# Optimization experiments

Measured on AMD Instinct MI355X. Metric: run time of the kernel, lower is better.

Reference implementation:

```python
import jax, jax.numpy as jnp
import numpy as np
from jax import lax

B, T, C = 4, 2048, 2048
HK, HV = 16, 16
DK, DV = 128, 128
KW = 4  # conv kernel width
KEY_DIM = HK * DK      # 2048
VAL_DIM = HV * DV      # 2048
QKV_DIM = 2 * KEY_DIM + VAL_DIM  # 6144
EPS_RMS = 1e-6
EPS_NORM = 1e-12


def setup_inputs() -> dict:
    key = jax.random.key(0)
    ks = jax.random.split(key, 7)
    s = 0.02
    x = jax.random.normal(ks[0], (B, T, C), dtype=jnp.float32)
    positions = jnp.broadcast_to(jnp.arange(T, dtype=jnp.int64 if jax.config.jax_enable_x64 else jnp.int32), (B, T))
    W_qkvz = jax.random.normal(ks[1], (C, QKV_DIM + VAL_DIM), dtype=jnp.float32) * s
    W_b = jax.random.normal(ks[2], (C, HV), dtype=jnp.float32) * s
    W_a = jax.random.normal(ks[3], (C, HV), dtype=jnp.float32) * s
    conv_w = jax.random.normal(ks[4], (QKV_DIM, 1, KW), dtype=jnp.float32) * 0.1
    norm_w = jnp.ones((DV,), dtype=jnp.float32)
    W_out = jax.random.normal(ks[5], (VAL_DIM, C), dtype=jnp.float32) * s
    return {"x": x, "positions": positions, "W_qkvz": W_qkvz, "W_b": W_b,
            "W_a": W_a, "conv_w": conv_w, "norm_w": norm_w, "W_out": W_out}


def _l2norm(u):
    n = jnp.sqrt(jnp.sum(u * u, axis=-1, keepdims=True))
    return u / jnp.maximum(n, EPS_NORM)


def _forward(x, W_qkvz, W_b, W_a, conv_w, norm_w, W_out):
    qkvz = x @ W_qkvz                               # [B,T,QKV+VAL]
    qkv, z = qkvz[..., :QKV_DIM], qkvz[..., QKV_DIM:]
    z = z.reshape(B, T, HV, DV)
    beta = jax.nn.sigmoid(x @ W_b)                  # [B,T,HV]
    alpha = jax.nn.sigmoid(x @ W_a)                 # [B,T,HV]

    # depthwise causal conv1d (padding K-1 then truncate to T)
    xc = jnp.transpose(qkv, (0, 2, 1))              # [B,QKV_DIM,T]
    xc = lax.conv_general_dilated(xc, conv_w, window_strides=(1,),
                                  padding=[(KW - 1, 0)],
                                  feature_group_count=QKV_DIM,
                                  dimension_numbers=("NCH", "OIH", "NCH"))
    qkv = jnp.transpose(jax.nn.silu(xc), (0, 2, 1))  # [B,T,QKV_DIM]

    q = _l2norm(qkv[..., :KEY_DIM].reshape(B, T, HK, DK))
    k = _l2norm(qkv[..., KEY_DIM:2 * KEY_DIM].reshape(B, T, HK, DK))
    v = qkv[..., 2 * KEY_DIM:].reshape(B, T, HV, DV)

    def step(state, inp):
        q_t, k_t, v_t, b_t, a_t = inp               # [B,H,DK],[B,H,DK],[B,H,DV],[B,H],[B,H]
        state = a_t[:, :, None, None] * state + \
                b_t[:, :, None, None] * (k_t[..., :, None] * v_t[:, :, None, :])
        out = jnp.einsum('bhk,bhkv->bhv', q_t, state)
        return state, out

    state0 = jnp.zeros((B, HK, DK, DV), dtype=x.dtype)
    seq = (jnp.moveaxis(q, 1, 0), jnp.moveaxis(k, 1, 0), jnp.moveaxis(v, 1, 0),
           jnp.moveaxis(beta, 1, 0), jnp.moveaxis(alpha, 1, 0))
    _, outs = lax.scan(step, state0, seq)           # [T,B,H,DV]
    out = jnp.moveaxis(outs, 0, 1)                  # [B,T,H,DV]

    # RMSNorm over head_v_dim (fp32), gated by sigmoid(z)
    of = out.astype(jnp.float32)
    rms = jnp.mean(of * of, axis=-1, keepdims=True)
    out = ((of * lax.rsqrt(rms + EPS_RMS)) * norm_w).astype(out.dtype)
    out = out * jax.nn.sigmoid(z)
    return out.reshape(B, T, VAL_DIM) @ W_out


def reference(x, positions, W_qkvz, W_b, W_a, conv_w, norm_w, W_out):
    return _forward(x, W_qkvz, W_b, W_a, conv_w, norm_w, W_out)
```

## Files before the change

kernel.cpp:

```cpp
#include <hip/hip_runtime.h>
#include <hip/hip_bf16.h>

typedef __bf16 bf16_t;
typedef __attribute__((ext_vector_type(8))) __bf16 bf16x8;
typedef __attribute__((ext_vector_type(4))) float floatx4;


__device__ __forceinline__ void gload16(const void* g, void* l) {
  __builtin_amdgcn_global_load_lds(
      (const __attribute__((address_space(1))) void*)g,
      (__attribute__((address_space(3))) void*)l, 16, 0, 0);
}

__global__ __launch_bounds__(256) void k_cast_bf16(const float* __restrict__ in,
                                                   bf16_t* __restrict__ out) {
  long i = ((long)blockIdx.x * 256 + threadIdx.x) * 8;
  const float4 a = *(const float4*)(in + i);
  const float4 b = *(const float4*)(in + i + 4);
  bf16x8 o;
  o[0] = (bf16_t)a.x; o[1] = (bf16_t)a.y; o[2] = (bf16_t)a.z; o[3] = (bf16_t)a.w;
  o[4] = (bf16_t)b.x; o[5] = (bf16_t)b.y; o[6] = (bf16_t)b.z; o[7] = (bf16_t)b.w;
  *(bf16x8*)(out + i) = o;
}

__global__ void k_transpose_cast(const float* __restrict__ in, bf16_t* __restrict__ out,
                                 int R, int Ccols) {
  __shared__ float tile[32][33];
  int c0 = blockIdx.x * 32, r0 = blockIdx.y * 32;
  for (int i = threadIdx.y; i < 32; i += 8)
    tile[i][threadIdx.x] = in[(long)(r0 + i) * Ccols + c0 + threadIdx.x];
  __syncthreads();
  for (int i = threadIdx.y; i < 32; i += 8)
    out[(long)(c0 + i) * R + r0 + threadIdx.x] = (bf16_t)tile[threadIdx.x][i];
}

__global__ void k_transpose_f32(const float* __restrict__ in, float* __restrict__ out,
                                int R, int Ccols) {
  int r = blockIdx.x * blockDim.x + threadIdx.x;
  if (r < R)
    for (int c = 0; c < Ccols; ++c) out[(long)c * R + r] = in[(long)r * Ccols + c];
}

__global__ __launch_bounds__(256) void k_beta_alpha(const float* __restrict__ x,
                                                    const float* __restrict__ WbT,
                                                    const float* __restrict__ WaT,
                                                    float* __restrict__ beta,
                                                    float* __restrict__ alpha) {
  extern __shared__ float xs[];
  const long row0 = (long)blockIdx.x * 16;
  const int tid = threadIdx.x;
  {
    const float4* src = (const float4*)(x + row0 * 2048);
    float4* dst = (float4*)xs;
    for (int i = tid; i < 16 * 512; i += 256) dst[i] = src[i];
  }
  __syncthreads();
  const int wv = tid >> 6, lane = tid & 63;
  for (int oo = 0; oo < 8; ++oo) {
    const int o = wv * 8 + oo;
    const float* Wrow = (o < 16) ? (WbT + (long)o * 2048) : (WaT + (long)(o - 16) * 2048);
    float acc[16];
#pragma unroll
    for (int r = 0; r < 16; ++r) acc[r] = 0.f;
    for (int kc = 0; kc < 8; ++kc) {
      const float4 w4 = *(const float4*)(Wrow + kc * 256 + lane * 4);
#pragma unroll
      for (int r = 0; r < 16; ++r) {
        const float4 xv = *(const float4*)&xs[r * 2048 + kc * 256 + lane * 4];
        acc[r] += w4.x * xv.x + w4.y * xv.y + w4.z * xv.z + w4.w * xv.w;
      }
    }
#pragma unroll
    for (int r = 0; r < 16; ++r) {
      float s = acc[r];
      for (int off = 32; off; off >>= 1) s += __shfl_down(s, off);
      if (lane == 0) {
        const long row = row0 + r;
        const int b = (int)(row >> 11), t = (int)(row & 2047);
        const float sig = 1.f / (1.f + __expf(-s));
        float* dst = (o < 16) ? beta : alpha;
        dst[((long)(b * 16 + (o & 15))) * 2048 + t] = sig;
      }
    }
  }
}

template <typename OUT_T>
__global__ __launch_bounds__(512, 2) void k_gemm256(const bf16_t* __restrict__ A,
                                                    const bf16_t* __restrict__ Bt,
                                                    OUT_T* __restrict__ C,
                                                    int N, int K, int lda) {
  extern __shared__ char gsm[];
  const int m0 = blockIdx.y * 256, n0 = blockIdx.x * 256;
  const int tid = threadIdx.x;
  const int w = tid >> 6, l = tid & 63;
  const int wm = w >> 2, wn = w & 3;
  const int l15 = l & 15, lg = l >> 4;

  const bf16_t* asrc[4];
  const bf16_t* bsrc[4];
  int dofs[4];
#pragma unroll
  for (int t = 0; t < 4; ++t) {
    int c = t * 512 + tid;
    int row = c >> 3, cs = (c & 7) ^ (row & 7);
    asrc[t] = A + (long)(m0 + row) * lda + cs * 8;
    bsrc[t] = Bt + (long)(n0 + row) * K + cs * 8;
    dofs[t] = c * 16;
  }

  auto STAGE = [&](int buf, int k0) {
    char* ab = gsm + buf * 65536;
    char* bb = ab + 32768;
#pragma unroll
    for (int t = 0; t < 4; ++t) {
      gload16(asrc[t] + k0, ab + dofs[t]);
      gload16(bsrc[t] + k0, bb + dofs[t]);
    }
  };

  floatx4 acc[8][4] = {};
  STAGE(0, 0);
  const int NK = K >> 6;
  for (int kt = 0; kt < NK; ++kt) {
    __syncthreads();
    if (kt + 1 < NK) STAGE((kt + 1) & 1, (kt + 1) << 6);
    const char* As_ = gsm + (kt & 1) * 65536;
    const char* Bs_ = As_ + 32768;
#pragma unroll
    for (int ks = 0; ks < 2; ++ks) {
      bf16x8 af[8], bfr[4];
#pragma unroll
      for (int mi = 0; mi < 8; ++mi) {
        const int r = wm * 128 + mi * 16 + l15;
        af[mi] = *(const bf16x8*)(As_ + r * 128 + ((((ks << 2) + lg) ^ (r & 7)) << 4));
      }
#pragma unroll
      for (int ni = 0; ni < 4; ++ni) {
        const int r = wn * 64 + ni * 16 + l15;
        bfr[ni] = *(const bf16x8*)(Bs_ + r * 128 + ((((ks << 2) + lg) ^ (r & 7)) << 4));
      }
      __builtin_amdgcn_s_setprio(1);
#pragma unroll
      for (int mi = 0; mi < 8; ++mi)
#pragma unroll
        for (int ni = 0; ni < 4; ++ni)
          acc[mi][ni] = __builtin_amdgcn_mfma_f32_16x16x32_bf16(af[mi], bfr[ni], acc[mi][ni], 0, 0, 0);
      __builtin_amdgcn_s_setprio(0);
    }
  }
  const int crow0 = m0 + wm * 128 + lg * 4;
  const int ccol = n0 + wn * 64 + l15;
#pragma unroll
  for (int mi = 0; mi < 8; ++mi)
#pragma unroll
    for (int ni = 0; ni < 4; ++ni)
#pragma unroll
      for (int r = 0; r < 4; ++r)
        C[(long)(crow0 + mi * 16 + r) * N + ccol + ni * 16] = (OUT_T)acc[mi][ni][r];
}

__global__ __launch_bounds__(256) void k_conv(const bf16_t* __restrict__ qkvz,
                                              const float* __restrict__ conv_w,
                                              bf16_t* __restrict__ q, bf16_t* __restrict__ k,
                                              bf16_t* __restrict__ v) {
  int row = blockIdx.x;
  int b = row >> 11, t = row & 2047;
  __shared__ float ys[6144];
  __shared__ float gsum[32][9];
  __shared__ float norms[32];
  const int c0 = threadIdx.x * 8;
  for (int c8 = c0; c8 < 6144; c8 += 2048) {
    bf16x8 xr[4];
#pragma unroll
    for (int w2 = 0; w2 < 4; ++w2) {
      int tt = t - 3 + w2;
      bf16x8 zr = {};
      xr[w2] = (tt >= 0) ? *(const bf16x8*)&qkvz[((long)(b * 2048 + tt)) * 8192 + c8] : zr;
    }
#pragma unroll
    for (int j = 0; j < 8; ++j) {
      float4 wv = *(const float4*)&conv_w[(c8 + j) * 4];
      float a = (float)xr[0][j] * wv.x + (float)xr[1][j] * wv.y +
                (float)xr[2][j] * wv.z + (float)xr[3][j] * wv.w;
      ys[c8 + j] = a / (1.f + __expf(-a));
    }
  }
  __syncthreads();
  {
    int g = threadIdx.x >> 3, j = threadIdx.x & 7;
    float s = 0.f;
#pragma unroll
    for (int e = 0; e < 16; ++e) {
      float yv = ys[g * 128 + j * 16 + e];
      s += yv * yv;
    }
    gsum[g][j] = s;
  }
  __syncthreads();
  if (threadIdx.x < 32) {
    float s = 0.f;
#pragma unroll
    for (int j = 0; j < 8; j++) s += gsum[threadIdx.x][j];
    norms[threadIdx.x] = 1.f / fmaxf(sqrtf(s), 1e-12f);
  }
  __syncthreads();
  for (int c8 = c0; c8 < 6144; c8 += 2048) {
    float scale;
    bf16_t* dst;
    if (c8 < 2048) {
      int h = c8 >> 7;
      scale = norms[h];
      dst = q + (((long)(b * 16 + h)) * 2048 + t) * 128 + (c8 & 127);
    } else if (c8 < 4096) {
      int h = (c8 - 2048) >> 7;
      scale = norms[16 + h];
      dst = k + (((long)(b * 16 + h)) * 2048 + t) * 128 + (c8 & 127);
    } else {
      scale = 1.f;
      int h = (c8 - 4096) >> 7;
      dst = v + (((long)(b * 16 + h)) * 2048 + t) * 128 + (c8 & 127);
    }
    bf16x8 o;
#pragma unroll
    for (int j = 0; j < 8; ++j) o[j] = (bf16_t)(ys[c8 + j] * scale);
    *(bf16x8*)dst = o;
  }
}

__global__ __launch_bounds__(256) void k_tr_kv(const bf16_t* __restrict__ kv,
                                               const bf16_t* __restrict__ vv,
                                               bf16_t* __restrict__ qkvz) {
  __shared__ bf16_t t_lds[64 * 136];
  int bh = blockIdx.x >> 5, tc = blockIdx.x & 31;
  int t0 = tc * 64;
  int tid = threadIdx.x;
#pragma unroll
  for (int pass = 0; pass < 2; ++pass) {
    const bf16_t* src = (pass == 0 ? kv : vv) + (long)bh * 2048 * 128 + (long)t0 * 128;
    int r = tid >> 2, sc = (tid & 3) * 32;
    bf16x8 x0 = *(const bf16x8*)(src + (long)r * 128 + sc);
    bf16x8 x1 = *(const bf16x8*)(src + (long)r * 128 + sc + 8);
    bf16x8 x2 = *(const bf16x8*)(src + (long)r * 128 + sc + 16);
    bf16x8 x3 = *(const bf16x8*)(src + (long)r * 128 + sc + 24);
    __syncthreads();
    *(bf16x8*)&t_lds[r * 136 + sc] = x0;
    *(bf16x8*)&t_lds[r * 136 + sc + 8] = x1;
    *(bf16x8*)&t_lds[r * 136 + sc + 16] = x2;
    *(bf16x8*)&t_lds[r * 136 + sc + 24] = x3;
    __syncthreads();
    int d = tid >> 1, h2 = tid & 1;
    bf16_t* dst = qkvz + (long)(bh * 128 + d) * 8192 + (pass ? 4096 : 2048) + t0 + h2 * 32;
#pragma unroll
    for (int g = 0; g < 4; ++g) {
      bf16x8 o;
#pragma unroll
      for (int j = 0; j < 8; ++j) o[j] = t_lds[(h2 * 32 + g * 8 + j) * 136 + d];
      *(bf16x8*)(dst + g * 8) = o;
    }
  }
}

__global__ __launch_bounds__(512, 1) void k_scan_chunked(
    const bf16_t* __restrict__ qv, const bf16_t* __restrict__ kv,
    bf16_t* __restrict__ qkvz, float* __restrict__ so_hi,
    const float* __restrict__ beta, const float* __restrict__ alpha) {
  extern __shared__ char smem[];
  bf16_t* q_lds = (bf16_t*)smem;
  bf16_t* kn_lds = q_lds + 8704;
  bf16_t* kT_lds = kn_lds + 8704;
  bf16_t* vT_lds = kT_lds + 9216;
  bf16_t* P_lds = vT_lds + 2304;
  bf16_t* St_lds = P_lds + 4608;
  float* G_lds = (float*)(St_lds + 4352);
  float* bet_lds = G_lds + 64;
  float* w_lds = bet_lds + 64;
  float* eG_lds = w_lds + 64;

  const int bh = blockIdx.x, dvb = blockIdx.y;
  const int b = bh >> 4, h = bh & 15;
  const int tid = threadIdx.x;
  const int w = tid >> 6, l = tid & 63;
  const int l15 = l & 15, lg = l >> 4;
  const int g = w & 1, r = w >> 1;

  const bf16_t* qb = qv + (long)bh * 2048 * 128;
  const bf16_t* kb = kv + (long)bh * 2048 * 128;
  const bf16_t* kTg = qkvz + (long)bh * 128 * 8192 + 2048;
  const bf16_t* vTg = qkvz + (long)(bh * 128 + dvb * 32) * 8192 + 4096;
  const float* bet = beta + (long)bh * 2048;
  const float* alp = alpha + (long)bh * 2048;

  floatx4 streg[2] = {};
  for (int i = tid; i < 2176; i += 512) ((float*)St_lds)[i] = 0.f;
  __syncthreads();

  const int sr = tid >> 3, ssc = (tid & 7) * 16;
  const int sdk = tid >> 2, ssc2 = (tid & 3) * 16;
  const int svr = tid >> 3, svc = (tid & 7) * 8;

  bf16x8 ra0, ra1, rb0, rb1, rc0, rc1, rd0 = {};
  float rbet = 0.f, ralp = 1.f;
  {
    const bf16_t* qs = qb + (long)sr * 128 + ssc;
    const bf16_t* ks = kb + (long)sr * 128 + ssc;
    const bf16_t* kts = kTg + (long)sdk * 8192 + ssc2;
    ra0 = *(const bf16x8*)qs; ra1 = *(const bf16x8*)(qs + 8);
    rb0 = *(const bf16x8*)ks; rb1 = *(const bf16x8*)(ks + 8);
    rc0 = *(const bf16x8*)kts; rc1 = *(const bf16x8*)(kts + 8);
    if (tid < 256) rd0 = *(const bf16x8*)(vTg + (long)svr * 8192 + svc);
    if (w == 0) { rbet = bet[l]; ralp = alp[l]; }
  }

  for (int c = 0; c < 32; ++c) {
    const int t0 = c * 64;
    {
      *(bf16x8*)&q_lds[sr * 136 + ssc] = ra0;
      *(bf16x8*)&q_lds[sr * 136 + ssc + 8] = ra1;
      *(bf16x8*)&kn_lds[sr * 136 + ssc] = rb0;
      *(bf16x8*)&kn_lds[sr * 136 + ssc + 8] = rb1;
      *(bf16x8*)&kT_lds[sdk * 72 + ssc2] = rc0;
      *(bf16x8*)&kT_lds[sdk * 72 + ssc2 + 8] = rc1;
      if (tid < 256) *(bf16x8*)&vT_lds[svr * 72 + svc] = rd0;
      if (w == 0) {
        float bsv = rbet;
        float la = __logf(ralp);
#pragma unroll
        for (int off = 1; off < 64; off <<= 1) {
          float xup = __shfl_up(la, off);
          if (l >= off) la += xup;
        }
        float ge = __shfl(la, 63);
        G_lds[l] = la;
        bet_lds[l] = bsv;
        w_lds[l] = bsv * __expf(ge - la);
        eG_lds[l] = __expf(la);
      }
    }
    __syncthreads();

    if (c + 1 < 32) {
      const int t1 = t0 + 64;
      const bf16_t* qs = qb + (long)(t1 + sr) * 128 + ssc;
      const bf16_t* ks = kb + (long)(t1 + sr) * 128 + ssc;
      const bf16_t* kts = kTg + (long)sdk * 8192 + t1 + ssc2;
      ra0 = *(const bf16x8*)qs; ra1 = *(const bf16x8*)(qs + 8);
      rb0 = *(const bf16x8*)ks; rb1 = *(const bf16x8*)(ks + 8);
      rc0 = *(const bf16x8*)kts; rc1 = *(const bf16x8*)(kts + 8);
      if (tid < 256) rd0 = *(const bf16x8*)(vTg + (long)svr * 8192 + t1 + svc);
      if (w == 0) { rbet = bet[t1 + l]; ralp = alp[t1 + l]; }
    }

    {
      bf16_t* p = &kT_lds[sdk * 72 + ssc2];
      bf16x8 x0 = *(bf16x8*)p, x1 = *(bf16x8*)(p + 8);
#pragma unroll
      for (int j = 0; j < 8; j++) {
        x0[j] = (bf16_t)((float)x0[j] * w_lds[ssc2 + j]);
        x1[j] = (bf16_t)((float)x1[j] * w_lds[ssc2 + 8 + j]);
      }
      *(bf16x8*)p = x0;
      *(bf16x8*)(p + 8) = x1;
    }

    {
      const int mi = w >> 1;
      bf16x8 aq[4];
#pragma unroll
      for (int ks = 0; ks < 4; ks++)
        aq[ks] = *(bf16x8*)&q_lds[(mi * 16 + l15) * 136 + ks * 32 + lg * 8];
#pragma unroll
      for (int sn2 = 0; sn2 < 2; sn2++) {
        const int sn = (w & 1) * 2 + sn2;
        floatx4 sc_ = {0.f, 0.f, 0.f, 0.f};
#pragma unroll
        for (int ks = 0; ks < 4; ks++) {
          bf16x8 bk = *(bf16x8*)&kn_lds[(sn * 16 + l15) * 136 + ks * 32 + lg * 8];
          sc_ = __builtin_amdgcn_mfma_f32_16x16x32_bf16(aq[ks], bk, sc_, 0, 0, 0);
        }
        const int sl = sn * 16 + l15;
        const float gs = G_lds[sl], bs = bet_lds[sl];
#pragma unroll
        for (int rr = 0; rr < 4; rr++) {
          const int tl = mi * 16 + lg * 4 + rr;
          float val = (sl <= tl) ? sc_[rr] * __expf(G_lds[tl] - gs) * bs : 0.f;
          P_lds[tl * 72 + sl] = (bf16_t)val;
        }
      }
    }
    __syncthreads();

    floatx4 acco = {0.f, 0.f, 0.f, 0.f};
    {
      const int rloc = g * 16 + l15;
      bf16x8 av0 = *(bf16x8*)&vT_lds[rloc * 72 + lg * 8];
      bf16x8 av1 = *(bf16x8*)&vT_lds[rloc * 72 + 32 + lg * 8];
      floatx4 f = {0.f, 0.f, 0.f, 0.f};
#pragma unroll
      for (int ks = 0; ks < 4; ks++) {
        bf16x8 aq = *(bf16x8*)&q_lds[(r * 16 + l15) * 136 + ks * 32 + lg * 8];
        bf16x8 bs_ = *(bf16x8*)&St_lds[rloc * 136 + ks * 32 + lg * 8];
        f = __builtin_amdgcn_mfma_f32_16x16x32_bf16(aq, bs_, f, 0, 0, 0);
      }
#pragma unroll
      for (int rr = 0; rr < 4; rr++) f[rr] *= eG_lds[r * 16 + lg * 4 + rr];
#pragma unroll
      for (int ks2 = 0; ks2 < 2; ks2++) {
        bf16x8 ap = *(bf16x8*)&P_lds[(r * 16 + l15) * 72 + ks2 * 32 + lg * 8];
        f = __builtin_amdgcn_mfma_f32_16x16x32_bf16(ap, (ks2 == 0) ? av0 : av1, f, 0, 0, 0);
      }
      acco = f;
      const float dcv = eG_lds[63];
#pragma unroll
      for (int ni = 0; ni < 2; ni++) {
        const int ni2 = r * 2 + ni;
#pragma unroll
        for (int rr = 0; rr < 4; rr++) streg[ni][rr] *= dcv;
        bf16x8 bk0 = *(bf16x8*)&kT_lds[(ni2 * 16 + l15) * 72 + lg * 8];
        bf16x8 bk1 = *(bf16x8*)&kT_lds[(ni2 * 16 + l15) * 72 + 32 + lg * 8];
        streg[ni] = __builtin_amdgcn_mfma_f32_16x16x32_bf16(av0, bk0, streg[ni], 0, 0, 0);
        streg[ni] = __builtin_amdgcn_mfma_f32_16x16x32_bf16(av1, bk1, streg[ni], 0, 0, 0);
      }
    }
    __syncthreads();

#pragma unroll
    for (int ni = 0; ni < 2; ni++) {
      const int ni2 = r * 2 + ni;
#pragma unroll
      for (int rr = 0; rr < 4; rr++)
        St_lds[(g * 16 + lg * 4 + rr) * 136 + ni2 * 16 + l15] = (bf16_t)streg[ni][rr];
    }
    {
      const int dvg = dvb * 32 + g * 16 + l15;
      const int hcol = h * 128 + dvg;
#pragma unroll
      for (int rr = 0; rr < 4; rr++) {
        const int t = t0 + r * 16 + lg * 4 + rr;
        const long row = (long)b * 2048 + t;
        if (hcol < 1024)
          ((float*)qkvz)[row * 4096 + hcol] = acco[rr];
        else
          so_hi[row * 1024 + hcol - 1024] = acco[rr];
      }
    }
  }
}

__global__ __launch_bounds__(256) void k_rmsgate(const float* __restrict__ so_hi,
                                                 const bf16_t* __restrict__ qkvz,
                                                 bf16_t* __restrict__ A2,
                                                 const float* __restrict__ norm_w) {
  long row = blockIdx.x;
  int tid = threadIdx.x;
  int h = tid >> 4, j = tid & 15;
  const float* srow = (h < 8) ? (const float*)qkvz + row * 4096 + h * 128 + j * 8
                              : so_hi + row * 1024 + (h - 8) * 128 + j * 8;
  float xv[8];
  *(float4*)&xv[0] = *(const float4*)srow;
  *(float4*)&xv[4] = *(const float4*)(srow + 4);
  float ss = 0.f;
#pragma unroll
  for (int e = 0; e < 8; e++) ss += xv[e] * xv[e];
  ss += __shfl_xor(ss, 1); ss += __shfl_xor(ss, 2);
  ss += __shfl_xor(ss, 4); ss += __shfl_xor(ss, 8);
  float rinv = rsqrtf(ss * (1.0f / 128.0f) + 1e-6f);
  const bf16_t* zrow = qkvz + row * 8192 + 6144 + h * 128 + j * 8;
  bf16x8 zv = *(const bf16x8*)zrow;
  bf16x8 o;
#pragma unroll
  for (int e = 0; e < 8; e++) {
    float z = (float)zv[e];
    float gate = 1.f / (1.f + __expf(-z));
    o[e] = (bf16_t)(xv[e] * rinv * norm_w[j * 8 + e] * gate);
  }
  *(bf16x8*)(A2 + row * 2048 + h * 128 + j * 8) = o;
}

extern "C" void kernel_launch(void* const* d_in, const int* in_sizes, int n_in,
                              void* d_out, int out_size, void* d_ws, size_t ws_size,
                              hipStream_t stream) {
  const float* x      = (const float*)d_in[0];
  const float* W_qkvz = (const float*)d_in[2];
  const float* W_b    = (const float*)d_in[3];
  const float* W_a    = (const float*)d_in[4];
  const float* conv_w = (const float*)d_in[5];
  const float* norm_w = (const float*)d_in[6];
  const float* W_out  = (const float*)d_in[7];
  float* out = (float*)d_out;
  char* ws = (char*)d_ws;

  bf16_t* qkvz  = (bf16_t*)(ws + 0);
  bf16_t* xb    = (bf16_t*)(ws + 134217728);
  bf16_t* qv    = (bf16_t*)(ws + 134217728);
  bf16_t* A2    = (bf16_t*)(ws + 134217728);
  bf16_t* WqT   = (bf16_t*)(ws + 167772160);
  bf16_t* kv    = (bf16_t*)(ws + 167772160);
  bf16_t* vv    = (bf16_t*)(ws + 201326592);
  float*  so_hi = (float*)(ws + 201326592);
  bf16_t* WoT   = (bf16_t*)(ws + 234881024);
  float*  WbT   = (float*)(ws + 243269632);
  float*  WaT   = (float*)(ws + 243400704);
  float*  beta  = (float*)(ws + 243531776);
  float*  alpha = (float*)(ws + 244056064);

  if (ws_size < 244580352) return;

  k_cast_bf16<<<8192, 256, 0, stream>>>(x, xb);
  k_transpose_cast<<<dim3(8192 / 32, 2048 / 32), dim3(32, 8), 0, stream>>>(W_qkvz, WqT, 2048, 8192);
  k_transpose_cast<<<dim3(2048 / 32, 2048 / 32), dim3(32, 8), 0, stream>>>(W_out, WoT, 2048, 2048);
  k_transpose_f32<<<8, 256, 0, stream>>>(W_b, WbT, 2048, 16);
  k_transpose_f32<<<8, 256, 0, stream>>>(W_a, WaT, 2048, 16);
  k_beta_alpha<<<512, 256, 131072, stream>>>(x, WbT, WaT, beta, alpha);
  k_gemm256<bf16_t><<<dim3(32, 32), 512, 131072, stream>>>(xb, WqT, qkvz, 8192, 2048, 2048);
  k_conv<<<8192, 256, 0, stream>>>(qkvz, conv_w, qv, kv, vv);
  k_tr_kv<<<2048, 256, 0, stream>>>(kv, vv, qkvz);
  k_scan_chunked<<<dim3(64, 4), 512, 76800, stream>>>(qv, kv, qkvz, so_hi, beta, alpha);
  k_rmsgate<<<8192, 256, 0, stream>>>(so_hi, qkvz, A2, norm_w);
  k_gemm256<float><<<dim3(8, 32), 512, 131072, stream>>>(A2, WoT, out, 2048, 2048, 2048);
  (void)in_sizes; (void)n_in; (void)out_size;
}
```

Baseline: 821.8 us.

## Fuse x bf16 cast into beta/alpha kernel and batch GEMM LDS fragment loads

```diff
diff --git a/kernel.cpp b/kernel.cpp
--- a/kernel.cpp
+++ b/kernel.cpp
@@ -10,17 +10,6 @@
   __builtin_amdgcn_global_load_lds(
       (const __attribute__((address_space(1))) void*)g,
       (__attribute__((address_space(3))) void*)l, 16, 0, 0);
-}
-
-__global__ __launch_bounds__(256) void k_cast_bf16(const float* __restrict__ in,
-                                                   bf16_t* __restrict__ out) {
-  long i = ((long)blockIdx.x * 256 + threadIdx.x) * 8;
-  const float4 a = *(const float4*)(in + i);
-  const float4 b = *(const float4*)(in + i + 4);
-  bf16x8 o;
-  o[0] = (bf16_t)a.x; o[1] = (bf16_t)a.y; o[2] = (bf16_t)a.z; o[3] = (bf16_t)a.w;
-  o[4] = (bf16_t)b.x; o[5] = (bf16_t)b.y; o[6] = (bf16_t)b.z; o[7] = (bf16_t)b.w;
-  *(bf16x8*)(out + i) = o;
 }
 
 __global__ void k_transpose_cast(const float* __restrict__ in, bf16_t* __restrict__ out,
@@ -45,7 +34,8 @@
                                                     const float* __restrict__ WbT,
                                                     const float* __restrict__ WaT,
                                                     float* __restrict__ beta,
-                                                    float* __restrict__ alpha) {
+                                                    float* __restrict__ alpha,
+                                                    bf16_t* __restrict__ xb) {
   extern __shared__ float xs[];
   const long row0 = (long)blockIdx.x * 16;
   const int tid = threadIdx.x;
@@ -55,6 +45,17 @@
     for (int i = tid; i < 16 * 512; i += 256) dst[i] = src[i];
   }
   __syncthreads();
+  {
+    bf16_t* xbrow = xb + row0 * 2048;
+    for (int i = tid; i < 4096; i += 256) {
+      const float4 a = *(const float4*)&xs[i * 8];
+      const float4 b2 = *(const float4*)&xs[i * 8 + 4];
+      bf16x8 o;
+      o[0] = (bf16_t)a.x; o[1] = (bf16_t)a.y; o[2] = (bf16_t)a.z; o[3] = (bf16_t)a.w;
+      o[4] = (bf16_t)b2.x; o[5] = (bf16_t)b2.y; o[6] = (bf16_t)b2.z; o[7] = (bf16_t)b2.w;
+      *(bf16x8*)(xbrow + i * 8) = o;
+    }
+  }
   const int wv = tid >> 6, lane = tid & 63;
   for (int oo = 0; oo < 8; ++oo) {
     const int o = wv * 8 + oo;
@@ -127,27 +128,39 @@
     if (kt + 1 < NK) STAGE((kt + 1) & 1, (kt + 1) << 6);
     const char* As_ = gsm + (kt & 1) * 65536;
     const char* Bs_ = As_ + 32768;
-#pragma unroll
-    for (int ks = 0; ks < 2; ++ks) {
-      bf16x8 af[8], bfr[4];
-#pragma unroll
-      for (int mi = 0; mi < 8; ++mi) {
-        const int r = wm * 128 + mi * 16 + l15;
-        af[mi] = *(const bf16x8*)(As_ + r * 128 + ((((ks << 2) + lg) ^ (r & 7)) << 4));
-      }
-#pragma unroll
-      for (int ni = 0; ni < 4; ++ni) {
-        const int r = wn * 64 + ni * 16 + l15;
-        bfr[ni] = *(const bf16x8*)(Bs_ + r * 128 + ((((ks << 2) + lg) ^ (r & 7)) << 4));
-      }
-      __builtin_amdgcn_s_setprio(1);
-#pragma unroll
-      for (int mi = 0; mi < 8; ++mi)
-#pragma unroll
-        for (int ni = 0; ni < 4; ++ni)
-          acc[mi][ni] = __builtin_amdgcn_mfma_f32_16x16x32_bf16(af[mi], bfr[ni], acc[mi][ni], 0, 0, 0);
-      __builtin_amdgcn_s_setprio(0);
-    }
+    bf16x8 af0[8], bf0[4], af1[8], bf1[4];
+#pragma unroll
+    for (int mi = 0; mi < 8; ++mi) {
+      const int r = wm * 128 + mi * 16 + l15;
+      af0[mi] = *(const bf16x8*)(As_ + r * 128 + ((lg ^ (r & 7)) << 4));
+    }
+#pragma unroll
+    for (int ni = 0; ni < 4; ++ni) {
+      const int r = wn * 64 + ni * 16 + l15;
+      bf0[ni] = *(const bf16x8*)(Bs_ + r * 128 + ((lg ^ (r & 7)) << 4));
+    }
+#pragma unroll
+    for (int mi = 0; mi < 8; ++mi) {
+      const int r = wm * 128 + mi * 16 + l15;
+      af1[mi] = *(const bf16x8*)(As_ + r * 128 + (((4 + lg) ^ (r & 7)) << 4));
+    }
+#pragma unroll
+    for (int ni = 0; ni < 4; ++ni) {
+      const int r = wn * 64 + ni * 16 + l15;
+      bf1[ni] = *(const bf16x8*)(Bs_ + r * 128 + (((4 + lg) ^ (r & 7)) << 4));
+    }
+    __builtin_amdgcn_s_setprio(1);
+#pragma unroll
+    for (int mi = 0; mi < 8; ++mi)
+#pragma unroll
+      for (int ni = 0; ni < 4; ++ni)
+        acc[mi][ni] = __builtin_amdgcn_mfma_f32_16x16x32_bf16(af0[mi], bf0[ni], acc[mi][ni], 0, 0, 0);
+#pragma unroll
+    for (int mi = 0; mi < 8; ++mi)
+#pragma unroll
+      for (int ni = 0; ni < 4; ++ni)
+        acc[mi][ni] = __builtin_amdgcn_mfma_f32_16x16x32_bf16(af1[mi], bf1[ni], acc[mi][ni], 0, 0, 0);
+    __builtin_amdgcn_s_setprio(0);
   }
   const int crow0 = m0 + wm * 128 + lg * 4;
   const int ccol = n0 + wn * 64 + l15;
@@ -506,12 +519,11 @@
 
   if (ws_size < 244580352) return;
 
-  k_cast_bf16<<<8192, 256, 0, stream>>>(x, xb);
   k_transpose_cast<<<dim3(8192 / 32, 2048 / 32), dim3(32, 8), 0, stream>>>(W_qkvz, WqT, 2048, 8192);
   k_transpose_cast<<<dim3(2048 / 32, 2048 / 32), dim3(32, 8), 0, stream>>>(W_out, WoT, 2048, 2048);
   k_transpose_f32<<<8, 256, 0, stream>>>(W_b, WbT, 2048, 16);
   k_transpose_f32<<<8, 256, 0, stream>>>(W_a, WaT, 2048, 16);
-  k_beta_alpha<<<512, 256, 131072, stream>>>(x, WbT, WaT, beta, alpha);
+  k_beta_alpha<<<512, 256, 131072, stream>>>(x, WbT, WaT, beta, alpha, xb);
   k_gemm256<bf16_t><<<dim3(32, 32), 512, 131072, stream>>>(xb, WqT, qkvz, 8192, 2048, 2048);
   k_conv<<<8192, 256, 0, stream>>>(qkvz, conv_w, qv, kv, vv);
   k_tr_kv<<<2048, 256, 0, stream>>>(kv, vv, qkvz);
```

Measured after the change: 820.0 us. Within noise of the previous version (-0.2%).
